# Kernel optimization log

Measured on AMD Instinct MI355X. Metric: run time of the kernel, lower is better.

## Reference

```python
import jax, jax.numpy as jnp
import numpy as np

B, N, D = 4, 2048, 512
H = 8
DH = D // H
FF = 2 * D


def setup_inputs() -> dict:
    key = jax.random.key(0)
    ks = jax.random.split(key, 16)
    s = lambda fan_in: 1.0 / np.sqrt(fan_in)
    inp = {
        "x0": jax.random.normal(ks[0], (B, N, D), jnp.float32),
        "x1": jax.random.normal(ks[1], (B, N, D), jnp.float32),
        # projections (torch Linear: weight [out, in])
        "Wqk": jax.random.uniform(ks[2], (D, D), jnp.float32, -s(D), s(D)),
        "bqk": jax.random.uniform(ks[3], (D,), jnp.float32, -s(D), s(D)),
        "Wv": jax.random.uniform(ks[4], (D, D), jnp.float32, -s(D), s(D)),
        "bv": jax.random.uniform(ks[5], (D,), jnp.float32, -s(D), s(D)),
        "Wo": jax.random.uniform(ks[6], (D, D), jnp.float32, -s(D), s(D)),
        "bo": jax.random.uniform(ks[7], (D,), jnp.float32, -s(D), s(D)),
        # FFN: Linear(2D,2D) -> LayerNorm(2D) -> GELU -> Linear(2D,D)
        "Wf1": jax.random.uniform(ks[8], (FF, FF), jnp.float32, -s(FF), s(FF)),
        "bf1": jax.random.uniform(ks[9], (FF,), jnp.float32, -s(FF), s(FF)),
        "ln_g": jnp.ones((FF,), jnp.float32),
        "ln_b": jnp.zeros((FF,), jnp.float32),
        "Wf2": jax.random.uniform(ks[10], (D, FF), jnp.float32, -s(FF), s(FF)),
        "bf2": jax.random.uniform(ks[11], (D,), jnp.float32, -s(FF), s(FF)),
    }
    return inp


def _split_heads(t):
    # [B,N,D] -> [B,H,N,DH]
    return t.reshape(B, N, H, DH).transpose(0, 2, 1, 3)


def _attn(q, k, v):
    # q,k,v: [B,H,N,DH]; scale by sqrt(d_k) as in the torch Attention module
    scores = jnp.einsum("bhnd,bhmd->bhnm", q, k) / jnp.sqrt(jnp.float32(DH))
    attn = jax.nn.softmax(scores, axis=-1)
    return jnp.einsum("bhnm,bhmd->bhnd", attn, v)


def _merge_heads(t):
    # [B,H,N,DH] -> [B,N,D]
    return t.transpose(0, 2, 1, 3).reshape(B, N, D)


def _ffn(x, Wf1, bf1, ln_g, ln_b, Wf2, bf2):
    h = x @ Wf1.T + bf1
    mu = jnp.mean(h, axis=-1, keepdims=True)
    var = jnp.mean(jnp.square(h - mu), axis=-1, keepdims=True)
    h = (h - mu) / jnp.sqrt(var + 1e-5) * ln_g + ln_b
    h = jax.nn.gelu(h, approximate=False)
    return h @ Wf2.T + bf2


def reference(x0, x1, Wqk, bqk, Wv, bv, Wo, bo, Wf1, bf1, ln_g, ln_b, Wf2, bf2):
    qk0 = _split_heads(x0 @ Wqk.T + bqk)
    qk1 = _split_heads(x1 @ Wqk.T + bqk)
    v0 = _split_heads(x0 @ Wv.T + bv)
    v1 = _split_heads(x1 @ Wv.T + bv)

    m0 = _merge_heads(_attn(qk0, qk1, v1)) @ Wo.T + bo
    m1 = _merge_heads(_attn(qk1, qk0, v0)) @ Wo.T + bo

    y0 = x0 + _ffn(jnp.concatenate([x0, m0], -1), Wf1, bf1, ln_g, ln_b, Wf2, bf2)
    y1 = x1 + _ffn(jnp.concatenate([x1, m1], -1), Wf1, bf1, ln_g, ln_b, Wf2, bf2)
    return (y0, y1)
```

## Files before the change

### kernel.cpp

```cpp
#include <hip/hip_runtime.h>
#include <hip/hip_bf16.h>
#include <math.h>

typedef __bf16 bf16;
typedef __bf16 bf16x8 __attribute__((ext_vector_type(8)));
typedef __bf16 bf16x4 __attribute__((ext_vector_type(4)));
typedef float  f32x4  __attribute__((ext_vector_type(4)));
typedef float  f32x16 __attribute__((ext_vector_type(16)));
typedef unsigned int u32x2 __attribute__((ext_vector_type(2)));

#define DEVI __device__ __forceinline__

DEVI void async16(bf16* lds, const bf16* g) {
    __builtin_amdgcn_global_load_lds(
        (const __attribute__((address_space(1))) unsigned int*)g,
        (__attribute__((address_space(3))) unsigned int*)lds, 16, 0, 0);
}
DEVI f32x4 mfma16(bf16x8 a, bf16x8 b, f32x4 c) {
    return __builtin_amdgcn_mfma_f32_16x16x32_bf16(a, b, c, 0, 0, 0);
}
DEVI f32x16 mfma32(bf16x8 a, bf16x8 b, f32x16 c) {
    return __builtin_amdgcn_mfma_f32_32x32x16_bf16(a, b, c, 0, 0, 0);
}
DEVI unsigned cvtpk(float lo, float hi) {
    unsigned r;
    asm("v_cvt_pk_bf16_f32 %0, %1, %2" : "=v"(r) : "v"(lo), "v"(hi));
    return r;
}
DEVI void pl32(unsigned &a, unsigned &b) {
    u32x2 r = __builtin_amdgcn_permlane32_swap(a, b, false, false);
    a = r.x; b = r.y;
}
DEVI bf16x8 mk8(unsigned a0, unsigned a1, unsigned b0, unsigned b1) {
    union { unsigned u[4]; bf16x8 v; } U;
    U.u[0] = a0; U.u[1] = a1; U.u[2] = b0; U.u[3] = b1;
    return U.v;
}

__global__ __launch_bounds__(256) void prep(
    const float* __restrict__ x0, const float* __restrict__ x1, bf16* __restrict__ Xbf,
    const float* __restrict__ Wqk, const float* __restrict__ Wv,
    const float* __restrict__ Wf1, const float* __restrict__ Wf2,
    bf16* __restrict__ Wqkv, bf16* __restrict__ Wbig, bf16* __restrict__ Wf1Rb,
    bf16* __restrict__ Wf2b,
    const float* __restrict__ Wo, bf16* __restrict__ WoT,
    const float* __restrict__ bo, const float* __restrict__ bf1,
    float* __restrict__ bf1p)
{
    __shared__ float Ls[64][65];
    const int bid = blockIdx.x, t = threadIdx.x;
    if (bid < 8192) {
        long i = (long)bid * 256 + t;
        long r = i >> 7, c = (i & 127) * 4;
        const float* src = (r < 8192) ? (x0 + r * 512 + c) : (x1 + (r - 8192) * 512 + c);
        float4 v = *(const float4*)src;
        bf16x4 o;
        o[0] = (bf16)v.x; o[1] = (bf16)v.y; o[2] = (bf16)v.z; o[3] = (bf16)v.w;
        *(bf16x4*)(Xbf + r * 1024 + c) = o;
    } else if (bid < 10240) {
        long i = (long)(bid - 8192) * 256 + t;
        const float* s; bf16* d;
        if (i < 131072) {
            s = (i < 65536) ? Wqk + i * 4 : Wv + (i - 65536) * 4;
            d = Wqkv + i * 4;
        } else if (i < 393216) {
            long e = (i - 131072) * 4, r = e >> 10, c = e & 1023;
            s = Wf1 + e;
            d = (c < 512) ? (Wbig + r * 1024 + c) : (Wf1Rb + r * 512 + (c - 512));
        } else {
            s = Wf2 + (i - 393216) * 4;
            d = Wf2b + (i - 393216) * 4;
        }
        float4 v = *(const float4*)s;
        bf16x4 o;
        o[0] = (bf16)v.x; o[1] = (bf16)v.y; o[2] = (bf16)v.z; o[3] = (bf16)v.w;
        *(bf16x4*)d = o;
    } else if (bid < 10304) {
        const int bb = bid - 10240;
        const int bi = bb & 7, bj = bb >> 3;
        const int i0 = bi * 64, j0 = bj * 64;
        const int r0 = t >> 4, c4 = (t & 15) * 4;
#pragma unroll
        for (int it = 0; it < 4; it++) {
            int row = r0 + 16 * it;
            float4 v = *(const float4*)(Wo + (long)(i0 + row) * 512 + j0 + c4);
            Ls[row][c4] = v.x; Ls[row][c4 + 1] = v.y;
            Ls[row][c4 + 2] = v.z; Ls[row][c4 + 3] = v.w;
        }
        __syncthreads();
#pragma unroll
        for (int it = 0; it < 4; it++) {
            int orow = r0 + 16 * it;
            bf16x4 o;
#pragma unroll
            for (int k = 0; k < 4; k++) o[k] = (bf16)Ls[c4 + k][orow];
            *(bf16x4*)(WoT + (long)(j0 + orow) * 512 + i0 + c4) = o;
        }
    } else {
        const int w = t >> 6, lane = t & 63;
        const int row = (bid - 10304) * 4 + w;
        const float* rp = Wf1 + (long)row * 1024 + 512 + lane * 8;
        float4 a = *(const float4*)rp;
        float4 b = *(const float4*)(rp + 4);
        const float* bp = bo + lane * 8;
        float4 c = *(const float4*)bp;
        float4 d = *(const float4*)(bp + 4);
        float s = a.x * c.x + a.y * c.y + a.z * c.z + a.w * c.w +
                  b.x * d.x + b.y * d.y + b.z * d.z + b.w * d.w;
#pragma unroll
        for (int k = 1; k < 64; k <<= 1) s += __shfl_xor(s, k);
        if (lane == 0) bf1p[row] = bf1[row] + s;
    }
}

template <int MODE>
__global__ __launch_bounds__(256) void gemm_bt(
    const bf16* __restrict__ A, long lda,
    const bf16* __restrict__ B, long ldb,
    const float* __restrict__ bias,
    void* __restrict__ Cout, long ldc,
    const float* __restrict__ res0, const float* __restrict__ res1,
    const float* __restrict__ bias2, void* __restrict__ Cout2,
    int M, int N, int K, float scale)
{
    __shared__ bf16 As[128 * 64];
    __shared__ bf16 Bs[128 * 64];
    const int t = threadIdx.x;
    const int w = t >> 6, lane = t & 63, quad = lane >> 4, m15 = lane & 15;
    const int wm = w >> 1, wn = w & 1;
    const int nbx = N >> 7;
    const int xcd = blockIdx.x & 7, local = blockIdx.x >> 3;
    const int mtiles_per_xcd = (int)(gridDim.x >> 3) / nbx;
    const int by = xcd * mtiles_per_xcd + local / nbx;
    const int bx = local % nbx;
    const long m0 = (long)by * 128, n0 = (long)bx * 128;

    f32x4 acc[4][4] = {};

    for (int k0 = 0; k0 < K; k0 += 64) {
#pragma unroll
        for (int i = 0; i < 4; i++) {
            int idx = i * 256 + t, row = idx >> 3, p = idx & 7;
            int gc = k0 + ((p ^ (row & 7)) * 8);
            async16(As + idx * 8, A + (m0 + row) * lda + gc);
            async16(Bs + idx * 8, B + (n0 + row) * ldb + gc);
        }
        __syncthreads();
#pragma unroll
        for (int kk = 0; kk < 2; kk++) {
            bf16x8 af[4], bfr[4];
#pragma unroll
            for (int mt = 0; mt < 4; mt++) {
                int row = wm * 64 + mt * 16 + m15;
                af[mt] = *(const bf16x8*)(As + row * 64 + (((kk * 4 + quad) ^ (row & 7)) * 8));
            }
#pragma unroll
            for (int nt = 0; nt < 4; nt++) {
                int row = wn * 64 + nt * 16 + m15;
                bfr[nt] = *(const bf16x8*)(Bs + row * 64 + (((kk * 4 + quad) ^ (row & 7)) * 8));
            }
#pragma unroll
            for (int mt = 0; mt < 4; mt++)
#pragma unroll
                for (int nt = 0; nt < 4; nt++)
                    acc[mt][nt] = mfma16(af[mt], bfr[nt], acc[mt][nt]);
        }
        __syncthreads();
    }

#pragma unroll
    for (int nt = 0; nt < 4; nt++) {
        long col = n0 + wn * 64 + nt * 16 + m15;
#pragma unroll
        for (int mt = 0; mt < 4; mt++) {
            long row = m0 + wm * 64 + mt * 16 + quad * 4;
            if (MODE == 0) {
                bf16* C = (bf16*)Cout;
                float bs = bias[col];
#pragma unroll
                for (int r = 0; r < 4; r++)
                    C[(row + r) * ldc + col] = (bf16)(acc[mt][nt][r] + bs);
            } else if (MODE == 4) {
                bf16* C = (bf16*)Cout;
#pragma unroll
                for (int r = 0; r < 4; r++)
                    C[(row + r) * ldc + col] = (bf16)acc[mt][nt][r];
            } else {
                float* C = (float*)Cout;
                float bs = bias[col];
#pragma unroll
                for (int r = 0; r < 4; r++) {
                    long grow = row + r;
                    const float* rs = (grow < 8192) ? (res0 + grow * 512)
                                                    : (res1 + (grow - 8192) * 512);
                    C[grow * ldc + col] = acc[mt][nt][r] + bs + rs[col];
                }
            }
        }
    }
}

template <int MODE>
__global__ __launch_bounds__(512, 2) void pipe_gemm(
    const bf16* __restrict__ A, long lda,
    const bf16* __restrict__ B, long ldb,
    const float* __restrict__ bias,
    void* __restrict__ Cout, long ldc,
    const float* __restrict__ bias2, void* __restrict__ Cout2,
    int M, int N, int K, float scale)
{
    __shared__ bf16 lds[65536];
    bf16* As = lds;
    bf16* Bs = lds + 32768;

    const int t = threadIdx.x;
    const int w = t >> 6, lane = t & 63, quad = lane >> 4, m15 = lane & 15;
    const int wm = w >> 2, wn = w & 3;
    const int nbx = N >> 8;
    const int xcd = blockIdx.x & 7, local = blockIdx.x >> 3;
    const int mtiles_per_xcd = (int)(gridDim.x >> 3) / nbx;
    const int by = xcd * mtiles_per_xcd + local / nbx;
    const int bx = local % nbx;
    const long m0 = (long)by * 256, n0 = (long)bx * 256;
    const int nt = K >> 6;

    f32x4 acc[8][4] = {};

    auto stage = [&](int kt) {
        const int slot = kt & 1;
        bf16* Ad = As + slot * 16384;
        bf16* Bd = Bs + slot * 16384;
        const int k0 = kt * 64;
#pragma unroll
        for (int i = 0; i < 4; i++) {
            int idx = i * 512 + t, row = idx >> 3, p = idx & 7;
            int gc = k0 + ((p ^ (row & 7)) * 8);
            async16(Ad + idx * 8, A + (m0 + row) * lda + gc);
        }
#pragma unroll
        for (int i = 0; i < 4; i++) {
            int idx = i * 512 + t, row = idx >> 3, p = idx & 7;
            int gc = k0 + ((p ^ (row & 7)) * 8);
            async16(Bd + idx * 8, B + (n0 + row) * ldb + gc);
        }
    };

    stage(0);
    stage(1);

    for (int kt = 0; kt < nt; kt++) {
        if (kt + 1 < nt) {
            asm volatile("s_waitcnt vmcnt(8)" ::: "memory");
        } else {
            asm volatile("s_waitcnt vmcnt(0)" ::: "memory");
        }
        __builtin_amdgcn_s_barrier();
        __builtin_amdgcn_sched_barrier(0);

        const bf16* Asl = As + (kt & 1) * 16384;
        const bf16* Bsl = Bs + (kt & 1) * 16384;
#pragma unroll
        for (int ksub = 0; ksub < 2; ksub++) {
            bf16x8 af[8], bfr[4];
#pragma unroll
            for (int mf = 0; mf < 8; mf++) {
                int row = wm * 128 + mf * 16 + m15;
                af[mf] = *(const bf16x8*)(Asl + row * 64 + (((ksub * 4 + quad) ^ (row & 7)) * 8));
            }
#pragma unroll
            for (int nf = 0; nf < 4; nf++) {
                int row = wn * 64 + nf * 16 + m15;
                bfr[nf] = *(const bf16x8*)(Bsl + row * 64 + (((ksub * 4 + quad) ^ (row & 7)) * 8));
            }
            __builtin_amdgcn_s_setprio(1);
#pragma unroll
            for (int mf = 0; mf < 8; mf++)
#pragma unroll
                for (int nf = 0; nf < 4; nf++)
                    acc[mf][nf] = mfma16(af[mf], bfr[nf], acc[mf][nf]);
            __builtin_amdgcn_s_setprio(0);
        }

        __builtin_amdgcn_sched_barrier(0);
        __builtin_amdgcn_s_barrier();
        __builtin_amdgcn_sched_barrier(0);
        if (kt + 2 < nt) stage(kt + 2);
    }

#pragma unroll
    for (int nf = 0; nf < 4; nf++) {
        long col = n0 + wn * 64 + nf * 16 + m15;
#pragma unroll
        for (int mf = 0; mf < 8; mf++) {
            long row = m0 + wm * 128 + mf * 16 + quad * 4;
            if (MODE == 0) {
                bf16* C = (bf16*)Cout;
                float bs = bias[col];
#pragma unroll
                for (int r = 0; r < 4; r++)
                    C[(row + r) * ldc + col] = (bf16)(acc[mf][nf][r] + bs);
            } else {
                if (col < 512) {
                    bf16* C = (bf16*)Cout;
                    float bs = bias[col];
#pragma unroll
                    for (int r = 0; r < 4; r++)
                        C[(row + r) * ldc + col] = (bf16)((acc[mf][nf][r] + bs) * scale);
                } else {
                    bf16* V = (bf16*)Cout2;
                    long v = col - 512;
                    float bs = bias2[v];
                    bf16x4 pv;
#pragma unroll
                    for (int r = 0; r < 4; r++) pv[r] = (bf16)(acc[mf][nf][r] + bs);
                    *(bf16x4*)(V + v * 16384 + row) = pv;
                }
            }
        }
    }
}

__global__ __launch_bounds__(512, 2) void pipe_ffn2(
    const bf16* __restrict__ A, long lda,
    const bf16* __restrict__ B, long ldb,
    const float* __restrict__ bias,
    float* __restrict__ C, long ldc,
    const float* __restrict__ res0, const float* __restrict__ res1,
    int M, int N, int K)
{
    __shared__ bf16 lds[49152];
    bf16* As = lds;
    bf16* Bs = lds + 16384;

    const int t = threadIdx.x;
    const int w = t >> 6, lane = t & 63, quad = lane >> 4, m15 = lane & 15;
    const int wm = w >> 2, wn = w & 3;
    const int nbx = N >> 8;
    const int xcd = blockIdx.x & 7, local = blockIdx.x >> 3;
    const int mtiles_per_xcd = (int)(gridDim.x >> 3) / nbx;
    const int by = xcd * mtiles_per_xcd + local / nbx;
    const int bx = local % nbx;
    const long m0 = (long)by * 128, n0 = (long)bx * 256;
    const int nt = K >> 6;

    f32x4 acc[4][4] = {};

    auto stage = [&](int kt) {
        const int slot = kt & 1;
        bf16* Ad = As + slot * 8192;
        bf16* Bd = Bs + slot * 16384;
        const int k0 = kt * 64;
#pragma unroll
        for (int i = 0; i < 2; i++) {
            int idx = i * 512 + t, row = idx >> 3, p = idx & 7;
            int gc = k0 + ((p ^ (row & 7)) * 8);
            async16(Ad + idx * 8, A + (m0 + row) * lda + gc);
        }
#pragma unroll
        for (int i = 0; i < 4; i++) {
            int idx = i * 512 + t, row = idx >> 3, p = idx & 7;
            int gc = k0 + ((p ^ (row & 7)) * 8);
            async16(Bd + idx * 8, B + (n0 + row) * ldb + gc);
        }
    };

    stage(0);
    stage(1);

    for (int kt = 0; kt < nt; kt++) {
        if (kt + 1 < nt) {
            asm volatile("s_waitcnt vmcnt(6)" ::: "memory");
        } else {
            asm volatile("s_waitcnt vmcnt(0)" ::: "memory");
        }
        __builtin_amdgcn_s_barrier();
        __builtin_amdgcn_sched_barrier(0);

        const bf16* Asl = As + (kt & 1) * 8192;
        const bf16* Bsl = Bs + (kt & 1) * 16384;
#pragma unroll
        for (int ksub = 0; ksub < 2; ksub++) {
            bf16x8 af[4], bfr[4];
#pragma unroll
            for (int mf = 0; mf < 4; mf++) {
                int row = wm * 64 + mf * 16 + m15;
                af[mf] = *(const bf16x8*)(Asl + row * 64 + (((ksub * 4 + quad) ^ (row & 7)) * 8));
            }
#pragma unroll
            for (int nf = 0; nf < 4; nf++) {
                int row = wn * 64 + nf * 16 + m15;
                bfr[nf] = *(const bf16x8*)(Bsl + row * 64 + (((ksub * 4 + quad) ^ (row & 7)) * 8));
            }
            __builtin_amdgcn_s_setprio(1);
#pragma unroll
            for (int mf = 0; mf < 4; mf++)
#pragma unroll
                for (int nf = 0; nf < 4; nf++)
                    acc[mf][nf] = mfma16(af[mf], bfr[nf], acc[mf][nf]);
            __builtin_amdgcn_s_setprio(0);
        }

        __builtin_amdgcn_sched_barrier(0);
        __builtin_amdgcn_s_barrier();
        __builtin_amdgcn_sched_barrier(0);
        if (kt + 2 < nt) stage(kt + 2);
    }

#pragma unroll
    for (int nf = 0; nf < 4; nf++) {
        long col = n0 + wn * 64 + nf * 16 + m15;
        float bs = bias[col];
#pragma unroll
        for (int mf = 0; mf < 4; mf++) {
            long row = m0 + wm * 64 + mf * 16 + quad * 4;
#pragma unroll
            for (int r = 0; r < 4; r++) {
                long grow = row + r;
                const float* rs = (grow < 8192) ? (res0 + grow * 512)
                                                : (res1 + (grow - 8192) * 512);
                C[grow * ldc + col] = acc[mf][nf][r] + bs + rs[col];
            }
        }
    }
}

__global__ __launch_bounds__(256, 4) void flash_attn(const bf16* __restrict__ QK,
                                                     const bf16* __restrict__ VT,
                                                     bf16* __restrict__ o)
{
    __shared__ bf16 lds[20480];
    bf16* Ks = lds;
    bf16* Vs = lds + 8192;

    const int t = threadIdx.x, w = t >> 6, lane = t & 63;
    const int l31 = lane & 31, hi = lane >> 5;
    const int j = blockIdx.x;
    const int hs = j & 63;
    const int qt = j >> 6;
    const int h = hs & 7, b = (hs >> 3) & 3, dir = hs >> 5;
    const long qrow0  = (long)dir * 8192 + b * 2048 + qt * 128;
    const long kvrow0 = (long)(1 - dir) * 8192 + b * 2048;
    const int hc = h * 64;

#pragma unroll
    for (int i = 0; i < 4; i++) {
        int idx = i * 256 + t, row = idx >> 3, p = idx & 7;
        async16(lds + idx * 8, QK + (qrow0 + row) * 512 + hc + ((p ^ (row & 7)) * 8));
    }
    __syncthreads();
    bf16x8 qf[4];
    {
        int qrow = w * 32 + l31;
#pragma unroll
        for (int kd = 0; kd < 4; kd++)
            qf[kd] = *(const bf16x8*)(lds + qrow * 64 + (((kd * 2 + hi) ^ (qrow & 7)) * 8));
    }
    __syncthreads();

#pragma unroll
    for (int i = 0; i < 2; i++) {
        int idx = i * 256 + t, row = idx >> 3, p = idx & 7;
        async16(Ks + idx * 8, QK + (kvrow0 + row) * 512 + hc + ((p ^ (row & 7)) * 8));
    }
#pragma unroll
    for (int i = 0; i < 2; i++) {
        int idx = i * 256 + t, row = idx >> 3, p = idx & 7;
        async16(Vs + idx * 8, VT + (long)(hc + row) * 16384 + kvrow0 + ((p ^ (row & 7)) * 8));
    }

    f32x16 oacc[2] = {};
    f32x16 racc = {};
    f32x16 sP = {};
    bf16x8 ones;
#pragma unroll
    for (int k2 = 0; k2 < 8; k2++) ones[k2] = (bf16)1.0f;

    auto SM_PV = [&](f32x16 &s, const bf16* Vb, int ksbase) {
#pragma unroll
        for (int r = 0; r < 16; r++) s[r] = exp2f(s[r]);
#pragma unroll
        for (int sh = 0; sh < 2; sh++) {
            unsigned a0 = cvtpk(s[8 * sh + 0], s[8 * sh + 1]);
            unsigned a1 = cvtpk(s[8 * sh + 2], s[8 * sh + 3]);
            unsigned b0 = cvtpk(s[8 * sh + 4], s[8 * sh + 5]);
            unsigned b1 = cvtpk(s[8 * sh + 6], s[8 * sh + 7]);
            pl32(a0, b0); pl32(a1, b1);
            bf16x8 pa = mk8(a0, a1, b0, b1);
            const int ks = ksbase + sh;
            __builtin_amdgcn_s_setprio(1);
#pragma unroll
            for (int db = 0; db < 2; db++) {
                const int vrow = db * 32 + l31;
                bf16x8 vf = *(const bf16x8*)(Vb + vrow * 64 + (((ks * 2 + hi) ^ (vrow & 7)) * 8));
                oacc[db] = mfma32(pa, vf, oacc[db]);
            }
            racc = mfma32(pa, ones, racc);
            __builtin_amdgcn_s_setprio(0);
        }
    };

    for (int kb = 0; kb < 32; kb++) {
        bf16* Kc = Ks + (kb & 1) * 4096;
        bf16* Vc = Vs + (kb % 3) * 4096;
        const bf16* Vp = Vs + ((kb + 2) % 3) * 4096;

        asm volatile("s_waitcnt vmcnt(0)" ::: "memory");
        __builtin_amdgcn_s_barrier();

        if (kb < 31) {
            const long knext = kvrow0 + (kb + 1) * 64;
            bf16* Kn = Ks + ((kb + 1) & 1) * 4096;
            bf16* Vn = Vs + ((kb + 1) % 3) * 4096;
#pragma unroll
            for (int i = 0; i < 2; i++) {
                int idx = i * 256 + t, row = idx >> 3, p = idx & 7;
                async16(Kn + idx * 8, QK + (knext + row) * 512 + hc + ((p ^ (row & 7)) * 8));
            }
#pragma unroll
            for (int i = 0; i < 2; i++) {
                int idx = i * 256 + t, row = idx >> 3, p = idx & 7;
                async16(Vn + idx * 8, VT + (long)(hc + row) * 16384 + knext + ((p ^ (row & 7)) * 8));
            }
        }

        f32x16 sA = {};
        {
            const int krow = l31;
            const int ksw = krow & 7;
            bf16x8 kf0 = *(const bf16x8*)(Kc + krow * 64 + (((0 + hi) ^ ksw) * 8));
            bf16x8 kf1 = *(const bf16x8*)(Kc + krow * 64 + (((2 + hi) ^ ksw) * 8));
            bf16x8 kf2 = *(const bf16x8*)(Kc + krow * 64 + (((4 + hi) ^ ksw) * 8));
            bf16x8 kf3 = *(const bf16x8*)(Kc + krow * 64 + (((6 + hi) ^ ksw) * 8));
            __builtin_amdgcn_s_setprio(1);
            sA = mfma32(kf0, qf[0], sA);
            sA = mfma32(kf1, qf[1], sA);
            sA = mfma32(kf2, qf[2], sA);
            sA = mfma32(kf3, qf[3], sA);
            __builtin_amdgcn_s_setprio(0);
        }

        if (kb > 0) SM_PV(sP, Vp, 2);

        f32x16 sB = {};
        {
            const int krow = 32 + l31;
            const int ksw = krow & 7;
            bf16x8 kf0 = *(const bf16x8*)(Kc + krow * 64 + (((0 + hi) ^ ksw) * 8));
            bf16x8 kf1 = *(const bf16x8*)(Kc + krow * 64 + (((2 + hi) ^ ksw) * 8));
            bf16x8 kf2 = *(const bf16x8*)(Kc + krow * 64 + (((4 + hi) ^ ksw) * 8));
            bf16x8 kf3 = *(const bf16x8*)(Kc + krow * 64 + (((6 + hi) ^ ksw) * 8));
            __builtin_amdgcn_s_setprio(1);
            sB = mfma32(kf0, qf[0], sB);
            sB = mfma32(kf1, qf[1], sB);
            sB = mfma32(kf2, qf[2], sB);
            sB = mfma32(kf3, qf[3], sB);
            __builtin_amdgcn_s_setprio(0);
        }

        SM_PV(sA, Vc, 0);

        sP = sB;
    }
    SM_PV(sP, Vs + 4096, 2);

#pragma unroll
    for (int reg = 0; reg < 16; reg++) {
        const int q = (reg & 3) + 8 * (reg >> 2) + 4 * hi;
        const float inv = 1.f / racc[reg];
        const long row = qrow0 + w * 32 + q;
#pragma unroll
        for (int db = 0; db < 2; db++)
            o[row * 1024 + hc + db * 32 + l31] = (bf16)(oacc[db][reg] * inv);
    }
}

__global__ __launch_bounds__(256) void ln_gelu(bf16* __restrict__ H,
                                               const float* __restrict__ g,
                                               const float* __restrict__ bta)
{
    const int row = blockIdx.x, t = threadIdx.x;
    const int w = t >> 6, lane = t & 63;
    bf16* hp = H + (long)row * 1024 + t * 4;
    bf16x4 hv = *(const bf16x4*)hp;
    float h[4];
#pragma unroll
    for (int j = 0; j < 4; j++) h[j] = (float)hv[j];
    float s1 = h[0] + h[1] + h[2] + h[3];
    float s2 = h[0] * h[0] + h[1] * h[1] + h[2] * h[2] + h[3] * h[3];
#pragma unroll
    for (int d = 1; d < 64; d <<= 1) {
        s1 += __shfl_xor(s1, d);
        s2 += __shfl_xor(s2, d);
    }
    __shared__ float rbuf[8];
    if (lane == 0) { rbuf[w] = s1; rbuf[4 + w] = s2; }
    __syncthreads();
    s1 = rbuf[0] + rbuf[1] + rbuf[2] + rbuf[3];
    s2 = rbuf[4] + rbuf[5] + rbuf[6] + rbuf[7];
    const float mu = s1 * (1.f / 1024.f);
    const float var = s2 * (1.f / 1024.f) - mu * mu;
    const float rstd = rsqrtf(var + 1e-5f);
    bf16x4 out;
#pragma unroll
    for (int j = 0; j < 4; j++) {
        int c = t * 4 + j;
        float x = (h[j] - mu) * rstd * g[c] + bta[c];
        float y = 0.5f * x * (1.f + erff(x * 0.70710678118654752f));
        out[j] = (bf16)y;
    }
    *(bf16x4*)hp = out;
}

extern "C" void kernel_launch(void* const* d_in, const int* in_sizes, int n_in,
                              void* d_out, int out_size, void* d_ws, size_t ws_size,
                              hipStream_t stream)
{
    const float* x0  = (const float*)d_in[0];
    const float* x1  = (const float*)d_in[1];
    const float* Wqk = (const float*)d_in[2];
    const float* bqk = (const float*)d_in[3];
    const float* Wv  = (const float*)d_in[4];
    const float* bv  = (const float*)d_in[5];
    const float* Wo  = (const float*)d_in[6];
    const float* bo  = (const float*)d_in[7];
    const float* Wf1 = (const float*)d_in[8];
    const float* bf1 = (const float*)d_in[9];
    const float* lng = (const float*)d_in[10];
    const float* lnb = (const float*)d_in[11];
    const float* Wf2 = (const float*)d_in[12];
    const float* bf2 = (const float*)d_in[13];

    char* ws = (char*)d_ws;
    bf16* Xbf   = (bf16*)ws; ws += 16384L * 1024 * 2;
    bf16* QKbf  = (bf16*)ws;
    bf16* Hbuf  = (bf16*)ws;
    ws += 16384L * 512 * 2;
    bf16* VtG   = (bf16*)ws; ws += 16384L * 512 * 2;
    bf16* Wqkv  = (bf16*)ws; ws += 1024L * 512 * 2;
    bf16* Wbig  = (bf16*)ws; ws += 1024L * 1024 * 2;
    bf16* Wf1Rb = (bf16*)ws; ws += 1024L * 512 * 2;
    bf16* Wf2b  = (bf16*)ws; ws += 512L * 1024 * 2;
    bf16* WoT   = (bf16*)ws; ws += 512L * 512 * 2;
    float* bf1p = (float*)ws; ws += 1024 * 4;

    const float qs = 0.42466090014400953f;

    prep<<<10560, 256, 0, stream>>>(x0, x1, Xbf, Wqk, Wv, Wf1, Wf2,
                                    Wqkv, Wbig, Wf1Rb, Wf2b, Wo, WoT, bo, bf1, bf1p);

    gemm_bt<4><<<32, 256, 0, stream>>>(Wf1Rb, 512, WoT, 512, nullptr,
                                       Wbig + 512, 1024, nullptr, nullptr,
                                       nullptr, nullptr, 1024, 512, 512, 1.f);

    pipe_gemm<5><<<256, 512, 0, stream>>>(Xbf, 1024, Wqkv, 512, bqk,
                                          QKbf, 512, bv, VtG,
                                          16384, 1024, 512, qs);

    flash_attn<<<1024, 256, 0, stream>>>(QKbf, VtG, Xbf + 512);

    pipe_gemm<0><<<256, 512, 0, stream>>>(Xbf, 1024, Wbig, 1024, bf1p,
                                          Hbuf, 1024, nullptr, nullptr,
                                          16384, 1024, 1024, 1.f);
    ln_gelu<<<16384, 256, 0, stream>>>(Hbuf, lng, lnb);
    pipe_ffn2<<<256, 512, 0, stream>>>(Hbuf, 1024, Wf2b, 1024, bf2,
                                       (float*)d_out, 512, x0, x1,
                                       16384, 512, 1024);
}
```

Measured before the change: 360.7 us.

## Restructure GEMM k-loop barriers, simplify attention pipeline, add fast erf approximation

The two pipelined GEMM kernels now issue the second k-substep's LDS reads before the barrier and the next stage prefetch, so the MFMAs for that substep overlap the global loads. The attention kernel drops its three-buffer software-pipelined softmax/PV schedule in favour of a simpler double-buffered loop that handles both 32-row halves in sequence. This reduces LDS use but loses the overlap between QK and PV. The LN-GELU kernel replaces erff with an Abramowitz-Stegun polynomial approximation (about 1e-7 error), and unused epilogue modes are removed from one GEMM.

```diff
diff --git a/kernel.cpp b/kernel.cpp
--- a/kernel.cpp
+++ b/kernel.cpp
@@ -35,6 +35,17 @@
     union { unsigned u[4]; bf16x8 v; } U;
     U.u[0] = a0; U.u[1] = a1; U.u[2] = b0; U.u[3] = b1;
     return U.v;
+}
+DEVI float erf_fast(float x) {
+    float ax = fabsf(x);
+    float t = 1.f / (1.f + 0.3275911f * ax);
+    float y = t * (0.254829592f +
+              t * (-0.284496736f +
+              t * (1.421413741f +
+              t * (-1.453152027f + t * 1.061405429f))));
+    float e = __expf(-ax * ax);
+    float r = 1.f - y * e;
+    return (x < 0.f) ? -r : r;
 }
 
 __global__ __launch_bounds__(256) void prep(
@@ -174,27 +185,11 @@
 #pragma unroll
         for (int mt = 0; mt < 4; mt++) {
             long row = m0 + wm * 64 + mt * 16 + quad * 4;
-            if (MODE == 0) {
-                bf16* C = (bf16*)Cout;
-                float bs = bias[col];
-#pragma unroll
-                for (int r = 0; r < 4; r++)
-                    C[(row + r) * ldc + col] = (bf16)(acc[mt][nt][r] + bs);
-            } else if (MODE == 4) {
+            if (MODE == 4) {
                 bf16* C = (bf16*)Cout;
 #pragma unroll
                 for (int r = 0; r < 4; r++)
                     C[(row + r) * ldc + col] = (bf16)acc[mt][nt][r];
-            } else {
-                float* C = (float*)Cout;
-                float bs = bias[col];
-#pragma unroll
-                for (int r = 0; r < 4; r++) {
-                    long grow = row + r;
-                    const float* rs = (grow < 8192) ? (res0 + grow * 512)
-                                                    : (res1 + (grow - 8192) * 512);
-                    C[grow * ldc + col] = acc[mt][nt][r] + bs + rs[col];
-                }
             }
         }
     }
@@ -259,18 +254,18 @@
 
         const bf16* Asl = As + (kt & 1) * 16384;
         const bf16* Bsl = Bs + (kt & 1) * 16384;
-#pragma unroll
-        for (int ksub = 0; ksub < 2; ksub++) {
+
+        {
             bf16x8 af[8], bfr[4];
 #pragma unroll
             for (int mf = 0; mf < 8; mf++) {
                 int row = wm * 128 + mf * 16 + m15;
-                af[mf] = *(const bf16x8*)(Asl + row * 64 + (((ksub * 4 + quad) ^ (row & 7)) * 8));
+                af[mf] = *(const bf16x8*)(Asl + row * 64 + ((quad ^ (row & 7)) * 8));
             }
 #pragma unroll
             for (int nf = 0; nf < 4; nf++) {
                 int row = wn * 64 + nf * 16 + m15;
-                bfr[nf] = *(const bf16x8*)(Bsl + row * 64 + (((ksub * 4 + quad) ^ (row & 7)) * 8));
+                bfr[nf] = *(const bf16x8*)(Bsl + row * 64 + ((quad ^ (row & 7)) * 8));
             }
             __builtin_amdgcn_s_setprio(1);
 #pragma unroll
@@ -281,10 +276,31 @@
             __builtin_amdgcn_s_setprio(0);
         }
 
-        __builtin_amdgcn_sched_barrier(0);
-        __builtin_amdgcn_s_barrier();
-        __builtin_amdgcn_sched_barrier(0);
-        if (kt + 2 < nt) stage(kt + 2);
+        {
+            bf16x8 af[8], bfr[4];
+#pragma unroll
+            for (int mf = 0; mf < 8; mf++) {
+                int row = wm * 128 + mf * 16 + m15;
+                af[mf] = *(const bf16x8*)(Asl + row * 64 + (((4 + quad) ^ (row & 7)) * 8));
+            }
+#pragma unroll
+            for (int nf = 0; nf < 4; nf++) {
+                int row = wn * 64 + nf * 16 + m15;
+                bfr[nf] = *(const bf16x8*)(Bsl + row * 64 + (((4 + quad) ^ (row & 7)) * 8));
+            }
+            asm volatile("s_waitcnt lgkmcnt(0)" ::: "memory");
+            __builtin_amdgcn_sched_barrier(0);
+            __builtin_amdgcn_s_barrier();
+            __builtin_amdgcn_sched_barrier(0);
+            if (kt + 2 < nt) stage(kt + 2);
+            __builtin_amdgcn_s_setprio(1);
+#pragma unroll
+            for (int mf = 0; mf < 8; mf++)
+#pragma unroll
+                for (int nf = 0; nf < 4; nf++)
+                    acc[mf][nf] = mfma16(af[mf], bfr[nf], acc[mf][nf]);
+            __builtin_amdgcn_s_setprio(0);
+        }
     }
 
 #pragma unroll
@@ -378,18 +394,18 @@
 
         const bf16* Asl = As + (kt & 1) * 8192;
         const bf16* Bsl = Bs + (kt & 1) * 16384;
-#pragma unroll
-        for (int ksub = 0; ksub < 2; ksub++) {
+
+        {
             bf16x8 af[4], bfr[4];
 #pragma unroll
             for (int mf = 0; mf < 4; mf++) {
                 int row = wm * 64 + mf * 16 + m15;
-                af[mf] = *(const bf16x8*)(Asl + row * 64 + (((ksub * 4 + quad) ^ (row & 7)) * 8));
+                af[mf] = *(const bf16x8*)(Asl + row * 64 + ((quad ^ (row & 7)) * 8));
             }
 #pragma unroll
             for (int nf = 0; nf < 4; nf++) {
                 int row = wn * 64 + nf * 16 + m15;
-                bfr[nf] = *(const bf16x8*)(Bsl + row * 64 + (((ksub * 4 + quad) ^ (row & 7)) * 8));
+                bfr[nf] = *(const bf16x8*)(Bsl + row * 64 + ((quad ^ (row & 7)) * 8));
             }
             __builtin_amdgcn_s_setprio(1);
 #pragma unroll
@@ -400,10 +416,31 @@
             __builtin_amdgcn_s_setprio(0);
         }
 
-        __builtin_amdgcn_sched_barrier(0);
-        __builtin_amdgcn_s_barrier();
-        __builtin_amdgcn_sched_barrier(0);
-        if (kt + 2 < nt) stage(kt + 2);
+        {
+            bf16x8 af[4], bfr[4];
+#pragma unroll
+            for (int mf = 0; mf < 4; mf++) {
+                int row = wm * 64 + mf * 16 + m15;
+                af[mf] = *(const bf16x8*)(Asl + row * 64 + (((4 + quad) ^ (row & 7)) * 8));
+            }
+#pragma unroll
+            for (int nf = 0; nf < 4; nf++) {
+                int row = wn * 64 + nf * 16 + m15;
+                bfr[nf] = *(const bf16x8*)(Bsl + row * 64 + (((4 + quad) ^ (row & 7)) * 8));
+            }
+            asm volatile("s_waitcnt lgkmcnt(0)" ::: "memory");
+            __builtin_amdgcn_sched_barrier(0);
+            __builtin_amdgcn_s_barrier();
+            __builtin_amdgcn_sched_barrier(0);
+            if (kt + 2 < nt) stage(kt + 2);
+            __builtin_amdgcn_s_setprio(1);
+#pragma unroll
+            for (int mf = 0; mf < 4; mf++)
+#pragma unroll
+                for (int nf = 0; nf < 4; nf++)
+                    acc[mf][nf] = mfma16(af[mf], bfr[nf], acc[mf][nf]);
+            __builtin_amdgcn_s_setprio(0);
+        }
     }
 
 #pragma unroll
@@ -428,9 +465,7 @@
                                                      const bf16* __restrict__ VT,
                                                      bf16* __restrict__ o)
 {
-    __shared__ bf16 lds[20480];
-    bf16* Ks = lds;
-    bf16* Vs = lds + 8192;
+    __shared__ bf16 lds[16384];
 
     const int t = threadIdx.x, w = t >> 6, lane = t & 63;
     const int l31 = lane & 31, hi = lane >> 5;
@@ -460,57 +495,31 @@
 #pragma unroll
     for (int i = 0; i < 2; i++) {
         int idx = i * 256 + t, row = idx >> 3, p = idx & 7;
-        async16(Ks + idx * 8, QK + (kvrow0 + row) * 512 + hc + ((p ^ (row & 7)) * 8));
+        async16(lds + idx * 8, QK + (kvrow0 + row) * 512 + hc + ((p ^ (row & 7)) * 8));
     }
 #pragma unroll
     for (int i = 0; i < 2; i++) {
         int idx = i * 256 + t, row = idx >> 3, p = idx & 7;
-        async16(Vs + idx * 8, VT + (long)(hc + row) * 16384 + kvrow0 + ((p ^ (row & 7)) * 8));
+        async16(lds + 8192 + idx * 8, VT + (long)(hc + row) * 16384 + kvrow0 + ((p ^ (row & 7)) * 8));
     }
 
     f32x16 oacc[2] = {};
     f32x16 racc = {};
-    f32x16 sP = {};
     bf16x8 ones;
 #pragma unroll
-    for (int k2 = 0; k2 < 8; k2++) ones[k2] = (bf16)1.0f;
-
-    auto SM_PV = [&](f32x16 &s, const bf16* Vb, int ksbase) {
-#pragma unroll
-        for (int r = 0; r < 16; r++) s[r] = exp2f(s[r]);
-#pragma unroll
-        for (int sh = 0; sh < 2; sh++) {
-            unsigned a0 = cvtpk(s[8 * sh + 0], s[8 * sh + 1]);
-            unsigned a1 = cvtpk(s[8 * sh + 2], s[8 * sh + 3]);
-            unsigned b0 = cvtpk(s[8 * sh + 4], s[8 * sh + 5]);
-            unsigned b1 = cvtpk(s[8 * sh + 6], s[8 * sh + 7]);
-            pl32(a0, b0); pl32(a1, b1);
-            bf16x8 pa = mk8(a0, a1, b0, b1);
-            const int ks = ksbase + sh;
-            __builtin_amdgcn_s_setprio(1);
-#pragma unroll
-            for (int db = 0; db < 2; db++) {
-                const int vrow = db * 32 + l31;
-                bf16x8 vf = *(const bf16x8*)(Vb + vrow * 64 + (((ks * 2 + hi) ^ (vrow & 7)) * 8));
-                oacc[db] = mfma32(pa, vf, oacc[db]);
-            }
-            racc = mfma32(pa, ones, racc);
-            __builtin_amdgcn_s_setprio(0);
-        }
-    };
+    for (int k = 0; k < 8; k++) ones[k] = (bf16)1.0f;
 
     for (int kb = 0; kb < 32; kb++) {
-        bf16* Kc = Ks + (kb & 1) * 4096;
-        bf16* Vc = Vs + (kb % 3) * 4096;
-        const bf16* Vp = Vs + ((kb + 2) % 3) * 4096;
+        bf16* Kc = lds + (kb & 1) * 4096;
+        bf16* Vc = lds + 8192 + (kb & 1) * 4096;
 
         asm volatile("s_waitcnt vmcnt(0)" ::: "memory");
         __builtin_amdgcn_s_barrier();
 
         if (kb < 31) {
             const long knext = kvrow0 + (kb + 1) * 64;
-            bf16* Kn = Ks + ((kb + 1) & 1) * 4096;
-            bf16* Vn = Vs + ((kb + 1) % 3) * 4096;
+            bf16* Kn = lds + ((kb + 1) & 1) * 4096;
+            bf16* Vn = lds + 8192 + ((kb + 1) & 1) * 4096;
 #pragma unroll
             for (int i = 0; i < 2; i++) {
                 int idx = i * 256 + t, row = idx >> 3, p = idx & 7;
@@ -523,45 +532,48 @@
             }
         }
 
-        f32x16 sA = {};
-        {
-            const int krow = l31;
+#pragma unroll
+        for (int kb2 = 0; kb2 < 2; kb2++) {
+            const int krow = kb2 * 32 + l31;
             const int ksw = krow & 7;
             bf16x8 kf0 = *(const bf16x8*)(Kc + krow * 64 + (((0 + hi) ^ ksw) * 8));
             bf16x8 kf1 = *(const bf16x8*)(Kc + krow * 64 + (((2 + hi) ^ ksw) * 8));
             bf16x8 kf2 = *(const bf16x8*)(Kc + krow * 64 + (((4 + hi) ^ ksw) * 8));
             bf16x8 kf3 = *(const bf16x8*)(Kc + krow * 64 + (((6 + hi) ^ ksw) * 8));
+
+            f32x16 s0 = {};
             __builtin_amdgcn_s_setprio(1);
-            sA = mfma32(kf0, qf[0], sA);
-            sA = mfma32(kf1, qf[1], sA);
-            sA = mfma32(kf2, qf[2], sA);
-            sA = mfma32(kf3, qf[3], sA);
+            s0 = mfma32(kf0, qf[0], s0);
+            s0 = mfma32(kf1, qf[1], s0);
+            s0 = mfma32(kf2, qf[2], s0);
+            s0 = mfma32(kf3, qf[3], s0);
             __builtin_amdgcn_s_setprio(0);
-        }
-
-        if (kb > 0) SM_PV(sP, Vp, 2);
-
-        f32x16 sB = {};
-        {
-            const int krow = 32 + l31;
-            const int ksw = krow & 7;
-            bf16x8 kf0 = *(const bf16x8*)(Kc + krow * 64 + (((0 + hi) ^ ksw) * 8));
-            bf16x8 kf1 = *(const bf16x8*)(Kc + krow * 64 + (((2 + hi) ^ ksw) * 8));
-            bf16x8 kf2 = *(const bf16x8*)(Kc + krow * 64 + (((4 + hi) ^ ksw) * 8));
-            bf16x8 kf3 = *(const bf16x8*)(Kc + krow * 64 + (((6 + hi) ^ ksw) * 8));
-            __builtin_amdgcn_s_setprio(1);
-            sB = mfma32(kf0, qf[0], sB);
-            sB = mfma32(kf1, qf[1], sB);
-            sB = mfma32(kf2, qf[2], sB);
-            sB = mfma32(kf3, qf[3], sB);
-            __builtin_amdgcn_s_setprio(0);
-        }
-
-        SM_PV(sA, Vc, 0);
-
-        sP = sB;
-    }
-    SM_PV(sP, Vs + 4096, 2);
+
+#pragma unroll
+            for (int r = 0; r < 16; r++) s0[r] = exp2f(s0[r]);
+
+#pragma unroll
+            for (int sh = 0; sh < 2; sh++) {
+                const int ks = kb2 * 2 + sh;
+                unsigned a00 = cvtpk(s0[8 * sh + 0], s0[8 * sh + 1]);
+                unsigned a01 = cvtpk(s0[8 * sh + 2], s0[8 * sh + 3]);
+                unsigned b00 = cvtpk(s0[8 * sh + 4], s0[8 * sh + 5]);
+                unsigned b01 = cvtpk(s0[8 * sh + 6], s0[8 * sh + 7]);
+                pl32(a00, b00); pl32(a01, b01);
+                bf16x8 pa0 = mk8(a00, a01, b00, b01);
+
+                __builtin_amdgcn_s_setprio(1);
+#pragma unroll
+                for (int db = 0; db < 2; db++) {
+                    const int vrow = db * 32 + l31;
+                    bf16x8 vf = *(const bf16x8*)(Vc + vrow * 64 + (((ks * 2 + hi) ^ (vrow & 7)) * 8));
+                    oacc[db] = mfma32(pa0, vf, oacc[db]);
+                }
+                racc = mfma32(pa0, ones, racc);
+                __builtin_amdgcn_s_setprio(0);
+            }
+        }
+    }
 
 #pragma unroll
     for (int reg = 0; reg < 16; reg++) {
@@ -605,7 +617,7 @@
     for (int j = 0; j < 4; j++) {
         int c = t * 4 + j;
         float x = (h[j] - mu) * rstd * g[c] + bta[c];
-        float y = 0.5f * x * (1.f + erff(x * 0.70710678118654752f));
+        float y = 0.5f * x * (1.f + erf_fast(x * 0.70710678118654752f));
         out[j] = (bf16)y;
     }
     *(bf16x4*)hp = out;
```

Result: faster. 345.2 us (-4.3%).
